# Performance work log

Hardware: AMD Instinct MI355X
Metric: run time of the kernel (lower is better)

The kernel has to match this reference:

```python
import jax, jax.numpy as jnp
import numpy as np
import math

D_MODEL = 512
N_HEAD = 8
D_HEAD = 64
N_LAYER = 12
D_FF = 2048
EMB_SIZES = [32, 128, 256, 256, 32, 64]
N_TOKEN = [32, 32, 90, 70, 8, 8]
EPS_ATTN = 1e-6
EPS_LN = 1e-5


def _pos_encoding(seq, d):
    pos = np.arange(seq, dtype=np.float32)[:, None]
    div = np.exp(np.arange(0, d, 2, dtype=np.float32) * (-math.log(10000.0) / d))
    pe = np.zeros((seq, d), np.float32)
    pe[:, 0::2] = np.sin(pos * div)
    pe[:, 1::2] = np.cos(pos * div)
    return jnp.asarray(pe)


def _layernorm(x, g, b):
    mu = jnp.mean(x, axis=-1, keepdims=True)
    var = jnp.var(x, axis=-1, keepdims=True)
    return (x - mu) * jax.lax.rsqrt(var + EPS_LN) * g + b


def _phi(x):
    # elu(x) + 1
    return jnp.where(x > 0, x + 1.0, jnp.exp(x))


def _causal_linear_attention(h, wq, bq, wk, bk, wv, bv, wo, bo):
    B, S, _ = h.shape
    q = _phi((h @ wq + bq).reshape(B, S, N_HEAD, D_HEAD))
    k = _phi((h @ wk + bk).reshape(B, S, N_HEAD, D_HEAD))
    v = (h @ wv + bv).reshape(B, S, N_HEAD, D_HEAD)
    # cumulative K^T V state: [B,S,H,D,D]
    kv = jnp.cumsum(k[..., :, None] * v[..., None, :], axis=1)
    ksum = jnp.cumsum(k, axis=1)
    z = 1.0 / (jnp.einsum('bshd,bshd->bsh', q, ksum) + EPS_ATTN)
    out = jnp.einsum('bshd,bshde->bshe', q, kv) * z[..., None]
    return out.reshape(B, S, D_MODEL) @ wo + bo


def _forward(x, emb_bar, emb_position, emb_pitch, emb_duration, emb_type, emb_emotion,
             in_w, in_b, wq, bq, wk, bk, wv, bv, wo, bo,
             ln1_g, ln1_b, w1, b1, w2, b2, ln2_g, ln2_b,
             lnf_g, lnf_b, proj_emo_w, proj_emo_b):
    tables = [emb_bar, emb_position, emb_pitch, emb_duration, emb_type, emb_emotion]
    embs = jnp.concatenate(
        [jnp.take(t, x[..., i], axis=0) * math.sqrt(EMB_SIZES[i]) for i, t in enumerate(tables)],
        axis=-1)  # [B,S,768]
    h = embs @ in_w + in_b
    S = h.shape[1]
    h = h + _pos_encoding(S, D_MODEL)[None, :, :]  # dropout is identity in eval

    def layer(hc, p):
        (wq_, bq_, wk_, bk_, wv_, bv_, wo_, bo_,
         g1, be1, w1_, b1_, w2_, b2_, g2, be2) = p
        hc = hc + _causal_linear_attention(hc, wq_, bq_, wk_, bk_, wv_, bv_, wo_, bo_)
        hc = _layernorm(hc, g1, be1)
        y = jax.nn.gelu(hc @ w1_ + b1_, approximate=False) @ w2_ + b2_
        hc = _layernorm(hc + y, g2, be2)
        return hc, None

    params = (wq, bq, wk, bk, wv, bv, wo, bo, ln1_g, ln1_b, w1, b1, w2, b2, ln2_g, ln2_b)
    h, _ = jax.lax.scan(layer, h, params)
    h = _layernorm(h, lnf_g, lnf_b)  # final encoder norm
    y_emotion = h @ proj_emo_w + proj_emo_b
    return h, y_emotion


def setup_inputs() -> dict:
    key = jax.random.key(0)
    ks = jax.random.split(key, 16)
    B, S = 1, 1024
    x = jax.random.randint(ks[0], (B, S, 6), 0, 8)

    def lin(k, fin, fout):
        k1, k2 = jax.random.split(k)
        lim = 1.0 / np.sqrt(fin)
        return (jax.random.uniform(k1, (fin, fout), minval=-lim, maxval=lim),
                jax.random.uniform(k2, (fout,), minval=-lim, maxval=lim))

    def stack_lin(k, fin, fout):
        kk = jax.random.split(k, N_LAYER)
        ws, bs = zip(*[lin(kk[i], fin, fout) for i in range(N_LAYER)])
        return jnp.stack(ws), jnp.stack(bs)

    def stack_ln(val):
        return jnp.full((N_LAYER, D_MODEL), val, jnp.float32)

    inp = {'x': x}
    names = ['emb_bar', 'emb_position', 'emb_pitch', 'emb_duration', 'emb_type', 'emb_emotion']
    for i, n in enumerate(names):
        inp[n] = jax.random.normal(jax.random.fold_in(ks[1], i), (N_TOKEN[i], EMB_SIZES[i])) * 0.02
    inp['in_w'], inp['in_b'] = lin(ks[2], sum(EMB_SIZES), D_MODEL)
    inp['wq'], inp['bq'] = stack_lin(ks[3], D_MODEL, D_MODEL)
    inp['wk'], inp['bk'] = stack_lin(ks[4], D_MODEL, D_MODEL)
    inp['wv'], inp['bv'] = stack_lin(ks[5], D_MODEL, D_MODEL)
    inp['wo'], inp['bo'] = stack_lin(ks[6], D_MODEL, D_MODEL)
    inp['ln1_g'], inp['ln1_b'] = stack_ln(1.0), stack_ln(0.0)
    inp['w1'], inp['b1'] = stack_lin(ks[7], D_MODEL, D_FF)
    inp['w2'], inp['b2'] = stack_lin(ks[8], D_FF, D_MODEL)
    inp['ln2_g'], inp['ln2_b'] = stack_ln(1.0), stack_ln(0.0)
    inp['lnf_g'], inp['lnf_b'] = jnp.ones((D_MODEL,)), jnp.zeros((D_MODEL,))
    inp['proj_emo_w'], inp['proj_emo_b'] = lin(ks[9], D_MODEL, N_TOKEN[5])
    return inp


def reference(x, emb_bar, emb_position, emb_pitch, emb_duration, emb_type, emb_emotion,
              in_w, in_b, wq, bq, wk, bk, wv, bv, wo, bo,
              ln1_g, ln1_b, w1, b1, w2, b2, ln2_g, ln2_b,
              lnf_g, lnf_b, proj_emo_w, proj_emo_b):
    return _forward(x, emb_bar, emb_position, emb_pitch, emb_duration, emb_type, emb_emotion,
                    in_w, in_b, wq, bq, wk, bk, wv, bv, wo, bo,
                    ln1_g, ln1_b, w1, b1, w2, b2, ln2_g, ln2_b,
                    lnf_g, lnf_b, proj_emo_w, proj_emo_b)
```

## Files before the change

kernel.cpp:

```cpp
#include <hip/hip_runtime.h>
#include <hip/hip_bf16.h>
#include <math.h>


#define S_LEN 1024
#define DM 512
#define NH 8
#define DH 64
#define DFF 2048
#define NLAYER 12
#define CHUNK 64
#define NCH (S_LEN / CHUNK)

#define ACT_NONE 0
#define ACT_PHI  1
#define ACT_GELU 2

typedef short s16x8 __attribute__((ext_vector_type(8)));
typedef float f32x4 __attribute__((ext_vector_type(4)));

__device__ __forceinline__ short f2bf(float x) {
    __hip_bfloat16 h = __float2bfloat16(x);
    return *reinterpret_cast<short*>(&h);
}

__device__ __forceinline__ void fma4(f32x4& a, float s, const f32x4 v) {
    a.x = fmaf(s, v.x, a.x); a.y = fmaf(s, v.y, a.y);
    a.z = fmaf(s, v.z, a.z); a.w = fmaf(s, v.w, a.w);
}

__device__ __forceinline__ void tile_barrier() {
    asm volatile("s_waitcnt lgkmcnt(0)" ::: "memory");
    __builtin_amdgcn_s_barrier();
    asm volatile("" ::: "memory");
}

__global__ __launch_bounds__(256) void embed_kernel(
    const int* __restrict__ x,
    const float* __restrict__ t0, const float* __restrict__ t1,
    const float* __restrict__ t2, const float* __restrict__ t3,
    const float* __restrict__ t4, const float* __restrict__ t5,
    short* __restrict__ EMBb)
{
    int s = blockIdx.x;
    __shared__ int xi[6];
    if (threadIdx.x < 6) xi[threadIdx.x] = x[s * 6 + threadIdx.x];
    __syncthreads();
    for (int j = threadIdx.x; j < 768; j += 256) {
        int i, off, width; const float* t; float sc;
        if (j < 32)       { i = 0; off = 0;   t = t0; sc = 5.656854249f;  width = 32;  }
        else if (j < 160) { i = 1; off = 32;  t = t1; sc = 11.3137085f;   width = 128; }
        else if (j < 416) { i = 2; off = 160; t = t2; sc = 16.0f;         width = 256; }
        else if (j < 672) { i = 3; off = 416; t = t3; sc = 16.0f;         width = 256; }
        else if (j < 704) { i = 4; off = 672; t = t4; sc = 5.656854249f;  width = 32;  }
        else              { i = 5; off = 704; t = t5; sc = 8.0f;          width = 64;  }
        EMBb[s * 768 + j] = f2bf(t[xi[i] * width + (j - off)] * sc);
    }
}

__global__ __launch_bounds__(256) void transpose_w(
    const float* __restrict__ in, short* __restrict__ out, int K, int N)
{
    __shared__ short t[64][66];
    const int b = blockIdx.z;
    const int n0 = blockIdx.x * 64, k0 = blockIdx.y * 64;
    const float* ip = in + (size_t)b * K * N;
    short* op = out + (size_t)b * K * N;
    const int c = threadIdx.x & 63, r0 = (threadIdx.x >> 6) * 16;
    #pragma unroll
    for (int i = 0; i < 16; ++i)
        t[c][r0 + i] = f2bf(ip[(size_t)(k0 + r0 + i) * N + n0 + c]);
    __syncthreads();
    #pragma unroll
    for (int i = 0; i < 16; ++i)
        op[(size_t)(n0 + r0 + i) * K + k0 + c] = t[r0 + i][c];
}

__device__ __forceinline__ float apply_act(float v, int act) {
    if (act == ACT_PHI)       return (v > 0.0f) ? (v + 1.0f) : expf(v);
    else if (act == ACT_GELU) return 0.5f * v * (1.0f + erff(v * 0.70710678118654752f));
    return v;
}


__device__ __forceinline__ void ldswr64(short* lds, int srow, int scolb,
                                        const s16x8 r[2])
{
    const int bc = scolb ^ ((srow & 7) << 4);
    #pragma unroll
    for (int p = 0; p < 2; ++p)
        *(s16x8*)((char*)lds + (p * 32 + srow) * 128 + bc) = r[p];
}

__device__ __forceinline__ void compute64(
    const short* __restrict__ As, const short* __restrict__ Bs,
    int wr, int wc, int l15, int q, f32x4 acc[2][2])
{
    #pragma unroll
    for (int kh = 0; kh < 2; ++kh) {
        const int kb = kh * 64 + q * 16;
        s16x8 a[2], b[2];
        #pragma unroll
        for (int m = 0; m < 2; ++m) {
            int row = wr * 32 + m * 16 + l15;
            a[m] = *(const s16x8*)((const char*)As + row * 128 + (kb ^ ((row & 7) << 4)));
        }
        #pragma unroll
        for (int n = 0; n < 2; ++n) {
            int row = wc * 32 + n * 16 + l15;
            b[n] = *(const s16x8*)((const char*)Bs + row * 128 + (kb ^ ((row & 7) << 4)));
        }
        #pragma unroll
        for (int m = 0; m < 2; ++m)
            #pragma unroll
            for (int n = 0; n < 2; ++n)
                acc[m][n] = __builtin_amdgcn_mfma_f32_16x16x32_bf16(
                    a[m], b[n], acc[m][n], 0, 0, 0);
    }
}

__global__ __launch_bounds__(256) void gemm64(
    const short* __restrict__ A, const short* __restrict__ BT,
    const float* __restrict__ bias, const float* __restrict__ resid,
    float* __restrict__ Cf, short* __restrict__ Cbf,
    int N, int K, int act, int add_pe, int zparts)
{
    __shared__ short As[2][4096];
    __shared__ short Bs[2][4096];
    const int tid = threadIdx.x;
    const int row0 = blockIdx.y * 64, col0 = blockIdx.x * 64;
    const int z = blockIdx.z;
    const int Kz = K / zparts;
    const int kbase = z * Kz;
    const int w = tid >> 6, lane = tid & 63, q = lane >> 4, l15 = lane & 15;
    const int wr = w >> 1, wc = w & 1;
    const int nt = Kz >> 6;

    const int srow = tid >> 3;
    const int scolb = (tid & 7) * 16;
    const char* gA = (const char*)(A  + (size_t)(row0 + srow) * K + kbase) + scolb;
    const char* gB = (const char*)(BT + (size_t)(col0 + srow) * K + kbase) + scolb;
    const size_t rstep = (size_t)32 * K * 2;

    s16x8 ra[2], rb[2];
    #pragma unroll
    for (int p = 0; p < 2; ++p) {
        ra[p] = *(const s16x8*)(gA + p * rstep);
        rb[p] = *(const s16x8*)(gB + p * rstep);
    }
    ldswr64(As[0], srow, scolb, ra);
    ldswr64(Bs[0], srow, scolb, rb);
    if (nt > 1) {
        #pragma unroll
        for (int p = 0; p < 2; ++p) {
            ra[p] = *(const s16x8*)(gA + p * rstep + 128);
            rb[p] = *(const s16x8*)(gB + p * rstep + 128);
        }
    }
    tile_barrier();

    f32x4 acc[2][2] = {};
    int cur = 0;
    for (int t = 0; t < nt; ++t) {
        if (t + 1 < nt) {
            ldswr64(As[cur ^ 1], srow, scolb, ra);
            ldswr64(Bs[cur ^ 1], srow, scolb, rb);
        }
        if (t + 2 < nt) {
            size_t ko = (size_t)(t + 2) * 128;
            #pragma unroll
            for (int p = 0; p < 2; ++p) {
                ra[p] = *(const s16x8*)(gA + p * rstep + ko);
                rb[p] = *(const s16x8*)(gB + p * rstep + ko);
            }
        }
        compute64(As[cur], Bs[cur], wr, wc, l15, q, acc);
        tile_barrier();
        cur ^= 1;
    }

    if (zparts > 1 && Cf) Cf += (size_t)z * S_LEN * N;

    const int rbase = row0 + wr * 32 + q * 4;
    const int cbase = col0 + wc * 32 + l15;
    #pragma unroll
    for (int n = 0; n < 2; ++n) {
        int c = cbase + n * 16;
        float bia = (z == 0) ? bias[c] : 0.0f;
        #pragma unroll
        for (int m = 0; m < 2; ++m) {
            #pragma unroll
            for (int rg = 0; rg < 4; ++rg) {
                int r = rbase + m * 16 + rg;
                float v = apply_act(acc[m][n][rg] + bia, act);
                if (resid) v += resid[(size_t)r * N + c];
                if (add_pe) {
                    float freq = expf((float)(c & ~1) * (-9.210340371976184f / 512.0f));
                    float ang = (float)r * freq;
                    v += (c & 1) ? cosf(ang) : sinf(ang);
                }
                if (Cf)  Cf[(size_t)r * N + c] = v;
                if (Cbf) Cbf[(size_t)r * N + c] = f2bf(v);
            }
        }
    }
}

__global__ __launch_bounds__(256) void qkv64(
    const short* __restrict__ Hb,
    const short* __restrict__ qT, const short* __restrict__ kT, const short* __restrict__ vT,
    const float* __restrict__ bq, const float* __restrict__ bk, const float* __restrict__ bv,
    float* __restrict__ Qb, float* __restrict__ Kb, float* __restrict__ Vb)
{
    __shared__ short As[2][4096];
    __shared__ short Bs[2][4096];
    const int sel  = blockIdx.x >> 3;
    const int col0 = (blockIdx.x & 7) * 64;
    const int row0 = blockIdx.y * 64;
    const short* BT   = (sel == 0) ? qT : (sel == 1) ? kT : vT;
    const float* bias = (sel == 0) ? bq : (sel == 1) ? bk : bv;
    float* C          = (sel == 0) ? Qb : (sel == 1) ? Kb : Vb;
    const bool phi = (sel < 2);

    const int tid = threadIdx.x;
    const int w = tid >> 6, lane = tid & 63, q = lane >> 4, l15 = lane & 15;
    const int wr = w >> 1, wc = w & 1;

    const int srow = tid >> 3;
    const int scolb = (tid & 7) * 16;
    const char* gA = (const char*)(Hb + (size_t)(row0 + srow) * DM) + scolb;
    const char* gB = (const char*)(BT + (size_t)(col0 + srow) * DM) + scolb;
    const size_t rstep = (size_t)32 * DM * 2;

    s16x8 ra[2], rb[2];
    #pragma unroll
    for (int p = 0; p < 2; ++p) {
        ra[p] = *(const s16x8*)(gA + p * rstep);
        rb[p] = *(const s16x8*)(gB + p * rstep);
    }
    ldswr64(As[0], srow, scolb, ra);
    ldswr64(Bs[0], srow, scolb, rb);
    #pragma unroll
    for (int p = 0; p < 2; ++p) {
        ra[p] = *(const s16x8*)(gA + p * rstep + 128);
        rb[p] = *(const s16x8*)(gB + p * rstep + 128);
    }
    tile_barrier();

    f32x4 acc[2][2] = {};
    int cur = 0;
    for (int t = 0; t < 8; ++t) {
        if (t + 1 < 8) {
            ldswr64(As[cur ^ 1], srow, scolb, ra);
            ldswr64(Bs[cur ^ 1], srow, scolb, rb);
        }
        if (t + 2 < 8) {
            size_t ko = (size_t)(t + 2) * 128;
            #pragma unroll
            for (int p = 0; p < 2; ++p) {
                ra[p] = *(const s16x8*)(gA + p * rstep + ko);
                rb[p] = *(const s16x8*)(gB + p * rstep + ko);
            }
        }
        compute64(As[cur], Bs[cur], wr, wc, l15, q, acc);
        tile_barrier();
        cur ^= 1;
    }

    const int rbase = row0 + wr * 32 + q * 4;
    const int cbase = col0 + wc * 32 + l15;
    #pragma unroll
    for (int n = 0; n < 2; ++n) {
        int c = cbase + n * 16;
        float bia = bias[c];
        #pragma unroll
        for (int m = 0; m < 2; ++m) {
            #pragma unroll
            for (int rg = 0; rg < 4; ++rg) {
                int r = rbase + m * 16 + rg;
                float v = acc[m][n][rg] + bia;
                if (phi) v = (v > 0.0f) ? (v + 1.0f) : expf(v);
                C[(size_t)r * DM + c] = v;
            }
        }
    }
}

__global__ __launch_bounds__(256) void chunk_stats_kernel(
    const float* __restrict__ Kb, const float* __restrict__ Vb,
    float* __restrict__ KVC, float* __restrict__ KSC)
{
    const int h = blockIdx.x >> 4, c = blockIdx.x & 15;
    const int tid = threadIdx.x;
    __shared__ float Ks[64][68];
    __shared__ float Vs[64][68];
    #pragma unroll
    for (int it = 0; it < 4; ++it) {
        int j = tid + it * 256;
        int r = j >> 4, d0 = (j & 15) * 4;
        size_t g = (size_t)(c * CHUNK + r) * DM + h * 64 + d0;
        *(f32x4*)(&Ks[r][d0]) = *(const f32x4*)(Kb + g);
        *(f32x4*)(&Vs[r][d0]) = *(const f32x4*)(Vb + g);
    }
    __syncthreads();
    const int di = (tid >> 4) * 4, ei = (tid & 15) * 4;
    f32x4 a0 = {}, a1 = {}, a2 = {}, a3 = {}, ks = {};
    #pragma unroll 8
    for (int t = 0; t < 64; ++t) {
        f32x4 kk = *(const f32x4*)(&Ks[t][di]);
        f32x4 vv = *(const f32x4*)(&Vs[t][ei]);
        fma4(a0, kk.x, vv); fma4(a1, kk.y, vv);
        fma4(a2, kk.z, vv); fma4(a3, kk.w, vv);
        ks += kk;
    }
    float* out = KVC + (size_t)(c * NH + h) * 4096;
    *(f32x4*)(out + (size_t)(di + 0) * 64 + ei) = a0;
    *(f32x4*)(out + (size_t)(di + 1) * 64 + ei) = a1;
    *(f32x4*)(out + (size_t)(di + 2) * 64 + ei) = a2;
    *(f32x4*)(out + (size_t)(di + 3) * 64 + ei) = a3;
    if ((tid & 15) == 0)
        *(f32x4*)(KSC + (size_t)(c * NH + h) * 64 + di) = ks;
}

__global__ __launch_bounds__(256) void attn_out_kernel(
    const float* __restrict__ Qb, const float* __restrict__ Kb,
    const float* __restrict__ Vb, const float* __restrict__ KVC,
    const float* __restrict__ KSC, short* __restrict__ Ab)
{
    const int h = blockIdx.x >> 4, c = blockIdx.x & 15;
    const int tid = threadIdx.x;
    __shared__ float Qt[64][68];
    __shared__ float Kt[64][68];
    __shared__ float Vs[64][68];
    __shared__ float Ms[64][68];
    __shared__ float St[64][68];
    __shared__ float KSs[64];

    {
        f32x4 macc[4] = {};
        for (int cp = 0; cp < c; ++cp) {
            const float* src = KVC + (size_t)(cp * NH + h) * 4096;
            #pragma unroll
            for (int it = 0; it < 4; ++it)
                macc[it] += *(const f32x4*)(src + (size_t)(tid + it * 256) * 4);
        }
        #pragma unroll
        for (int it = 0; it < 4; ++it) {
            int j = tid + it * 256;
            *(f32x4*)(&Ms[j >> 4][(j & 15) * 4]) = macc[it];
        }
        if (tid < 64) {
            float s = 0.0f;
            for (int cp = 0; cp < c; ++cp)
                s += KSC[(size_t)(cp * NH + h) * 64 + tid];
            KSs[tid] = s;
        }
    }
    #pragma unroll
    for (int it = 0; it < 4; ++it) {
        int j = tid + it * 256;
        int r = j >> 4, d0 = (j & 15) * 4;
        size_t g = (size_t)(c * CHUNK + r) * DM + h * 64 + d0;
        f32x4 q = *(const f32x4*)(Qb + g);
        f32x4 k = *(const f32x4*)(Kb + g);
        f32x4 v = *(const f32x4*)(Vb + g);
        Qt[d0 + 0][r] = q.x; Qt[d0 + 1][r] = q.y; Qt[d0 + 2][r] = q.z; Qt[d0 + 3][r] = q.w;
        Kt[d0 + 0][r] = k.x; Kt[d0 + 1][r] = k.y; Kt[d0 + 2][r] = k.z; Kt[d0 + 3][r] = k.w;
        *(f32x4*)(&Vs[r][d0]) = v;
    }
    __syncthreads();

    const int si = tid >> 4, ti = tid & 15;
    const int s0 = si * 4, t0 = ti * 4;

    f32x4 accO0 = {}, accO1 = {}, accO2 = {}, accO3 = {};
    f32x4 den = {};
    #pragma unroll 8
    for (int d = 0; d < 64; ++d) {
        f32x4 qv = *(const f32x4*)(&Qt[d][s0]);
        f32x4 mv = *(const f32x4*)(&Ms[d][t0]);
        float ks = KSs[d];
        fma4(accO0, qv.x, mv); fma4(accO1, qv.y, mv);
        fma4(accO2, qv.z, mv); fma4(accO3, qv.w, mv);
        fma4(den, ks, qv);
    }

    f32x4 p0 = {}, p1 = {}, p2 = {}, p3 = {};
    if (ti <= si) {
        #pragma unroll 8
        for (int d = 0; d < 64; ++d) {
            f32x4 qv = *(const f32x4*)(&Qt[d][s0]);
            f32x4 kv = *(const f32x4*)(&Kt[d][t0]);
            fma4(p0, qv.x, kv); fma4(p1, qv.y, kv);
            fma4(p2, qv.z, kv); fma4(p3, qv.w, kv);
        }
        if (ti == si) {
            p0.y = 0.0f; p0.z = 0.0f; p0.w = 0.0f;
            p1.z = 0.0f; p1.w = 0.0f;
            p2.w = 0.0f;
        }
    }
    St[t0 + 0][s0 + 0] = p0.x; St[t0 + 1][s0 + 0] = p0.y;
    St[t0 + 2][s0 + 0] = p0.z; St[t0 + 3][s0 + 0] = p0.w;
    St[t0 + 0][s0 + 1] = p1.x; St[t0 + 1][s0 + 1] = p1.y;
    St[t0 + 2][s0 + 1] = p1.z; St[t0 + 3][s0 + 1] = p1.w;
    St[t0 + 0][s0 + 2] = p2.x; St[t0 + 1][s0 + 2] = p2.y;
    St[t0 + 2][s0 + 2] = p2.z; St[t0 + 3][s0 + 2] = p2.w;
    St[t0 + 0][s0 + 3] = p3.x; St[t0 + 1][s0 + 3] = p3.y;
    St[t0 + 2][s0 + 3] = p3.z; St[t0 + 3][s0 + 3] = p3.w;
    __syncthreads();

    const int tmax = s0 + 4;
    #pragma unroll 4
    for (int t2 = 0; t2 < tmax; ++t2) {
        f32x4 sv = *(const f32x4*)(&St[t2][s0]);
        f32x4 vv = *(const f32x4*)(&Vs[t2][t0]);
        fma4(accO0, sv.x, vv); fma4(accO1, sv.y, vv);
        fma4(accO2, sv.z, vv); fma4(accO3, sv.w, vv);
        den += sv;
    }

    short* op = Ab + (size_t)(c * CHUNK + s0) * DM + h * 64 + t0;
    {
        float z = 1.0f / (den.x + 1e-6f);
        short4 o; o.x = f2bf(accO0.x * z); o.y = f2bf(accO0.y * z);
        o.z = f2bf(accO0.z * z); o.w = f2bf(accO0.w * z);
        *reinterpret_cast<short4*>(op) = o;
    }
    {
        float z = 1.0f / (den.y + 1e-6f);
        short4 o; o.x = f2bf(accO1.x * z); o.y = f2bf(accO1.y * z);
        o.z = f2bf(accO1.z * z); o.w = f2bf(accO1.w * z);
        *reinterpret_cast<short4*>(op + DM) = o;
    }
    {
        float z = 1.0f / (den.z + 1e-6f);
        short4 o; o.x = f2bf(accO2.x * z); o.y = f2bf(accO2.y * z);
        o.z = f2bf(accO2.z * z); o.w = f2bf(accO2.w * z);
        *reinterpret_cast<short4*>(op + 2 * DM) = o;
    }
    {
        float z = 1.0f / (den.w + 1e-6f);
        short4 o; o.x = f2bf(accO3.x * z); o.y = f2bf(accO3.y * z);
        o.z = f2bf(accO3.z * z); o.w = f2bf(accO3.w * z);
        *reinterpret_cast<short4*>(op + 3 * DM) = o;
    }
}

__device__ __forceinline__ float block_reduce_sum(float v, float* smem)
{
    #pragma unroll
    for (int o = 32; o > 0; o >>= 1) v += __shfl_down(v, o, 64);
    int w = threadIdx.x >> 6;
    if ((threadIdx.x & 63) == 0) smem[w] = v;
    __syncthreads();
    v = smem[0] + smem[1] + smem[2] + smem[3];
    __syncthreads();
    return v;
}

__global__ __launch_bounds__(256) void ln_kernel(
    const float* __restrict__ X, const float* __restrict__ X2,
    const float* __restrict__ resid,
    const float* __restrict__ g, const float* __restrict__ b,
    float* __restrict__ O, short* __restrict__ Ob)
{
    __shared__ float red[4];
    const int row = blockIdx.x;
    const size_t base = (size_t)row * DM;
    const int t = threadIdx.x;
    float v0 = X[base + t], v1 = X[base + t + 256];
    if (X2)    { v0 += X2[base + t];    v1 += X2[base + t + 256]; }
    if (resid) { v0 += resid[base + t]; v1 += resid[base + t + 256]; }
    float mean = block_reduce_sum(v0 + v1, red) * (1.0f / 512.0f);
    float d0 = v0 - mean, d1 = v1 - mean;
    float var = block_reduce_sum(d0 * d0 + d1 * d1, red) * (1.0f / 512.0f);
    float rs = 1.0f / sqrtf(var + 1e-5f);
    float o0 = d0 * rs * g[t] + b[t];
    float o1 = d1 * rs * g[t + 256] + b[t + 256];
    O[base + t]       = o0;
    O[base + t + 256] = o1;
    if (Ob) {
        Ob[base + t]       = f2bf(o0);
        Ob[base + t + 256] = f2bf(o1);
    }
}

__global__ __launch_bounds__(256) void proj_emo_kernel(
    const float* __restrict__ HF, const float* __restrict__ pw,
    const float* __restrict__ pb, float* __restrict__ out)
{
    __shared__ float pws[4096];
    for (int i = threadIdx.x; i < 4096; i += 256) pws[i] = pw[i];
    __syncthreads();
    int idx = blockIdx.x * 256 + threadIdx.x;
    int r = idx >> 3, e = idx & 7;
    float acc = pb[e];
    const float* h = HF + (size_t)r * DM;
    for (int d = 0; d < DM; d += 4) {
        f32x4 hv = *(const f32x4*)(h + d);
        acc += hv.x * pws[(d + 0) * 8 + e] + hv.y * pws[(d + 1) * 8 + e]
             + hv.z * pws[(d + 2) * 8 + e] + hv.w * pws[(d + 3) * 8 + e];
    }
    out[idx] = acc;
}

extern "C" void kernel_launch(void* const* d_in, const int* in_sizes, int n_in,
                              void* d_out, int out_size, void* d_ws, size_t ws_size,
                              hipStream_t stream)
{
    const int*   x    = (const int*)d_in[0];
    const float* e0   = (const float*)d_in[1];
    const float* e1   = (const float*)d_in[2];
    const float* e2   = (const float*)d_in[3];
    const float* e3   = (const float*)d_in[4];
    const float* e4   = (const float*)d_in[5];
    const float* e5   = (const float*)d_in[6];
    const float* in_w = (const float*)d_in[7];
    const float* in_b = (const float*)d_in[8];
    const float* wq   = (const float*)d_in[9];
    const float* bq   = (const float*)d_in[10];
    const float* wk   = (const float*)d_in[11];
    const float* bk   = (const float*)d_in[12];
    const float* wv   = (const float*)d_in[13];
    const float* bv   = (const float*)d_in[14];
    const float* wo   = (const float*)d_in[15];
    const float* bo   = (const float*)d_in[16];
    const float* g1   = (const float*)d_in[17];
    const float* be1  = (const float*)d_in[18];
    const float* w1   = (const float*)d_in[19];
    const float* b1   = (const float*)d_in[20];
    const float* w2   = (const float*)d_in[21];
    const float* b2   = (const float*)d_in[22];
    const float* g2   = (const float*)d_in[23];
    const float* be2  = (const float*)d_in[24];
    const float* gf   = (const float*)d_in[25];
    const float* bfin = (const float*)d_in[26];
    const float* pw   = (const float*)d_in[27];
    const float* pb   = (const float*)d_in[28];
    float* outp = (float*)d_out;

    float* ws = (float*)d_ws;
    float* H    = ws;
    float* Y    = ws + 524288;
    float* Y2   = ws + 1048576;
    float* Qb   = ws + 1572864;
    float* Kb   = ws + 2097152;
    float* Vb   = ws + 2621440;
    float* KVC  = ws + 3145728;
    float* KSC  = ws + 3670016;
    short* sb   = (short*)(ws + 3678208);
    short* Hb   = sb;
    short* Ab   = sb + 524288;
    short* FFb  = sb + 1048576;
    short* EMBb = FFb;
    short* inT  = sb + 3145728;
    short* qT   = inT + 393216;
    short* kT   = qT + 3145728;
    short* vT   = kT + 3145728;
    short* oT   = vT + 3145728;
    short* w1T  = oT + 3145728;
    short* w2T  = w1T + 12582912;

    const dim3 blk256(256);

    transpose_w<<<dim3(8, 12, 1),  blk256, 0, stream>>>(in_w, inT, 768, DM);
    transpose_w<<<dim3(8, 8, 12),  blk256, 0, stream>>>(wq, qT, DM, DM);
    transpose_w<<<dim3(8, 8, 12),  blk256, 0, stream>>>(wk, kT, DM, DM);
    transpose_w<<<dim3(8, 8, 12),  blk256, 0, stream>>>(wv, vT, DM, DM);
    transpose_w<<<dim3(8, 8, 12),  blk256, 0, stream>>>(wo, oT, DM, DM);
    transpose_w<<<dim3(32, 8, 12), blk256, 0, stream>>>(w1, w1T, DM, DFF);
    transpose_w<<<dim3(8, 32, 12), blk256, 0, stream>>>(w2, w2T, DFF, DM);

    embed_kernel<<<S_LEN, blk256, 0, stream>>>(x, e0, e1, e2, e3, e4, e5, EMBb);
    gemm64<<<dim3(8, 16, 1), blk256, 0, stream>>>(EMBb, inT, in_b, nullptr,
                                                  H, Hb, DM, 768, ACT_NONE, 1, 1);

    for (int l = 0; l < NLAYER; ++l) {
        const short* qT_l = qT + (size_t)l * DM * DM;
        const short* kT_l = kT + (size_t)l * DM * DM;
        const short* vT_l = vT + (size_t)l * DM * DM;
        const short* oT_l = oT + (size_t)l * DM * DM;
        const short* w1T_l = w1T + (size_t)l * DM * DFF;
        const short* w2T_l = w2T + (size_t)l * DM * DFF;
        const float* bq_l = bq + l * DM;  const float* bk_l = bk + l * DM;
        const float* bv_l = bv + l * DM;  const float* bo_l = bo + l * DM;
        const float* b1_l = b1 + l * DFF; const float* b2_l = b2 + l * DM;

        qkv64<<<dim3(24, 16), blk256, 0, stream>>>(Hb, qT_l, kT_l, vT_l,
                                                   bq_l, bk_l, bv_l, Qb, Kb, Vb);

        chunk_stats_kernel<<<NCH * NH, blk256, 0, stream>>>(Kb, Vb, KVC, KSC);
        attn_out_kernel<<<NCH * NH, blk256, 0, stream>>>(Qb, Kb, Vb, KVC, KSC, Ab);

        gemm64<<<dim3(8, 16, 2), blk256, 0, stream>>>(Ab, oT_l, bo_l, nullptr,
                                                      Y, nullptr, DM, DM, ACT_NONE, 0, 2);
        ln_kernel<<<S_LEN, blk256, 0, stream>>>(Y, Y2, H,
                                                g1 + l * DM, be1 + l * DM, H, Hb);

        gemm64<<<dim3(32, 16, 1), blk256, 0, stream>>>(Hb, w1T_l, b1_l, nullptr,
                                                       nullptr, FFb, DFF, DM, ACT_GELU, 0, 1);
        gemm64<<<dim3(8, 16, 2), blk256, 0, stream>>>(FFb, w2T_l, b2_l, nullptr,
                                                      Y, nullptr, DM, DFF, ACT_NONE, 0, 2);
        ln_kernel<<<S_LEN, blk256, 0, stream>>>(Y, Y2, H,
                                                g2 + l * DM, be2 + l * DM, H, Hb);
    }

    ln_kernel<<<S_LEN, blk256, 0, stream>>>(H, nullptr, nullptr, gf, bfin, outp, nullptr);
    proj_emo_kernel<<<8192 / 256, blk256, 0, stream>>>(outp, pw, pb, outp + 524288);
}
```

Before: 1.057 ms.

## Use single-wave LayerNorm, merge QKVO weight transposes, reorder GEMM pipeline loop

LayerNorm now runs one 64-thread wave per row with vectorized float4 loads and xor-shuffle reductions, replacing the 256-thread block reduction and its LDS barriers. The four per-layer attention weight transposes are merged into one launch. The GEMM k-loops now compute before writing the next LDS buffer and skip the final barrier. The LDS write into the other buffer right after compute relies on the earlier barrier having ordered it against reads of that buffer, which is a subtle synchronisation risk.

```diff
diff --git a/kernel.cpp b/kernel.cpp
--- a/kernel.cpp
+++ b/kernel.cpp
@@ -76,6 +76,30 @@
         op[(size_t)(n0 + r0 + i) * K + k0 + c] = t[r0 + i][c];
 }
 
+__global__ __launch_bounds__(256) void transpose4_w(
+    const float* __restrict__ wA, const float* __restrict__ wB,
+    const float* __restrict__ wC, const float* __restrict__ wD,
+    short* __restrict__ oA, short* __restrict__ oB,
+    short* __restrict__ oC, short* __restrict__ oD)
+{
+    __shared__ short t[64][66];
+    const int zz = blockIdx.z;
+    const int which = zz & 3, b = zz >> 2;
+    const float* in = (which == 0) ? wA : (which == 1) ? wB : (which == 2) ? wC : wD;
+    short* out      = (which == 0) ? oA : (which == 1) ? oB : (which == 2) ? oC : oD;
+    const int n0 = blockIdx.x * 64, k0 = blockIdx.y * 64;
+    const float* ip = in + (size_t)b * DM * DM;
+    short* op = out + (size_t)b * DM * DM;
+    const int c = threadIdx.x & 63, r0 = (threadIdx.x >> 6) * 16;
+    #pragma unroll
+    for (int i = 0; i < 16; ++i)
+        t[c][r0 + i] = f2bf(ip[(size_t)(k0 + r0 + i) * DM + n0 + c]);
+    __syncthreads();
+    #pragma unroll
+    for (int i = 0; i < 16; ++i)
+        op[(size_t)(n0 + r0 + i) * DM + k0 + c] = t[r0 + i][c];
+}
+
 __device__ __forceinline__ float apply_act(float v, int act) {
     if (act == ACT_PHI)       return (v > 0.0f) ? (v + 1.0f) : expf(v);
     else if (act == ACT_GELU) return 0.5f * v * (1.0f + erff(v * 0.70710678118654752f));
@@ -162,20 +186,20 @@
     f32x4 acc[2][2] = {};
     int cur = 0;
     for (int t = 0; t < nt; ++t) {
+        compute64(As[cur], Bs[cur], wr, wc, l15, q, acc);
         if (t + 1 < nt) {
             ldswr64(As[cur ^ 1], srow, scolb, ra);
             ldswr64(Bs[cur ^ 1], srow, scolb, rb);
-        }
-        if (t + 2 < nt) {
-            size_t ko = (size_t)(t + 2) * 128;
-            #pragma unroll
-            for (int p = 0; p < 2; ++p) {
-                ra[p] = *(const s16x8*)(gA + p * rstep + ko);
-                rb[p] = *(const s16x8*)(gB + p * rstep + ko);
+            if (t + 2 < nt) {
+                size_t ko = (size_t)(t + 2) * 128;
+                #pragma unroll
+                for (int p = 0; p < 2; ++p) {
+                    ra[p] = *(const s16x8*)(gA + p * rstep + ko);
+                    rb[p] = *(const s16x8*)(gB + p * rstep + ko);
+                }
             }
-        }
-        compute64(As[cur], Bs[cur], wr, wc, l15, q, acc);
-        tile_barrier();
+            tile_barrier();
+        }
         cur ^= 1;
     }
 
@@ -250,20 +274,20 @@
     f32x4 acc[2][2] = {};
     int cur = 0;
     for (int t = 0; t < 8; ++t) {
+        compute64(As[cur], Bs[cur], wr, wc, l15, q, acc);
         if (t + 1 < 8) {
             ldswr64(As[cur ^ 1], srow, scolb, ra);
             ldswr64(Bs[cur ^ 1], srow, scolb, rb);
-        }
-        if (t + 2 < 8) {
-            size_t ko = (size_t)(t + 2) * 128;
-            #pragma unroll
-            for (int p = 0; p < 2; ++p) {
-                ra[p] = *(const s16x8*)(gA + p * rstep + ko);
-                rb[p] = *(const s16x8*)(gB + p * rstep + ko);
+            if (t + 2 < 8) {
+                size_t ko = (size_t)(t + 2) * 128;
+                #pragma unroll
+                for (int p = 0; p < 2; ++p) {
+                    ra[p] = *(const s16x8*)(gA + p * rstep + ko);
+                    rb[p] = *(const s16x8*)(gB + p * rstep + ko);
+                }
             }
-        }
-        compute64(As[cur], Bs[cur], wr, wc, l15, q, acc);
-        tile_barrier();
+            tile_barrier();
+        }
         cur ^= 1;
     }
 
@@ -447,42 +471,48 @@
     }
 }
 
-__device__ __forceinline__ float block_reduce_sum(float v, float* smem)
-{
-    #pragma unroll
-    for (int o = 32; o > 0; o >>= 1) v += __shfl_down(v, o, 64);
-    int w = threadIdx.x >> 6;
-    if ((threadIdx.x & 63) == 0) smem[w] = v;
-    __syncthreads();
-    v = smem[0] + smem[1] + smem[2] + smem[3];
-    __syncthreads();
-    return v;
-}
-
-__global__ __launch_bounds__(256) void ln_kernel(
+__global__ __launch_bounds__(64) void ln_kernel64(
     const float* __restrict__ X, const float* __restrict__ X2,
     const float* __restrict__ resid,
     const float* __restrict__ g, const float* __restrict__ b,
     float* __restrict__ O, short* __restrict__ Ob)
 {
-    __shared__ float red[4];
     const int row = blockIdx.x;
     const size_t base = (size_t)row * DM;
     const int t = threadIdx.x;
-    float v0 = X[base + t], v1 = X[base + t + 256];
-    if (X2)    { v0 += X2[base + t];    v1 += X2[base + t + 256]; }
-    if (resid) { v0 += resid[base + t]; v1 += resid[base + t + 256]; }
-    float mean = block_reduce_sum(v0 + v1, red) * (1.0f / 512.0f);
-    float d0 = v0 - mean, d1 = v1 - mean;
-    float var = block_reduce_sum(d0 * d0 + d1 * d1, red) * (1.0f / 512.0f);
+    const int i0 = 4 * t, i1 = 256 + 4 * t;
+    f32x4 v0 = *(const f32x4*)(X + base + i0);
+    f32x4 v1 = *(const f32x4*)(X + base + i1);
+    if (X2) {
+        v0 += *(const f32x4*)(X2 + base + i0);
+        v1 += *(const f32x4*)(X2 + base + i1);
+    }
+    if (resid) {
+        v0 += *(const f32x4*)(resid + base + i0);
+        v1 += *(const f32x4*)(resid + base + i1);
+    }
+    float s = v0.x + v0.y + v0.z + v0.w + v1.x + v1.y + v1.z + v1.w;
+    #pragma unroll
+    for (int m = 1; m < 64; m <<= 1) s += __shfl_xor(s, m, 64);
+    float mean = s * (1.0f / 512.0f);
+    f32x4 d0 = v0 - mean, d1 = v1 - mean;
+    float ss = d0.x * d0.x + d0.y * d0.y + d0.z * d0.z + d0.w * d0.w
+             + d1.x * d1.x + d1.y * d1.y + d1.z * d1.z + d1.w * d1.w;
+    #pragma unroll
+    for (int m = 1; m < 64; m <<= 1) ss += __shfl_xor(ss, m, 64);
+    float var = ss * (1.0f / 512.0f);
     float rs = 1.0f / sqrtf(var + 1e-5f);
-    float o0 = d0 * rs * g[t] + b[t];
-    float o1 = d1 * rs * g[t + 256] + b[t + 256];
-    O[base + t]       = o0;
-    O[base + t + 256] = o1;
+    f32x4 g0 = *(const f32x4*)(g + i0), g1v = *(const f32x4*)(g + i1);
+    f32x4 b0 = *(const f32x4*)(b + i0), b1v = *(const f32x4*)(b + i1);
+    f32x4 o0 = d0 * rs * g0 + b0;
+    f32x4 o1 = d1 * rs * g1v + b1v;
+    *(f32x4*)(O + base + i0) = o0;
+    *(f32x4*)(O + base + i1) = o1;
     if (Ob) {
-        Ob[base + t]       = f2bf(o0);
-        Ob[base + t + 256] = f2bf(o1);
+        short4 s0; s0.x = f2bf(o0.x); s0.y = f2bf(o0.y); s0.z = f2bf(o0.z); s0.w = f2bf(o0.w);
+        short4 s1; s1.x = f2bf(o1.x); s1.y = f2bf(o1.y); s1.z = f2bf(o1.z); s1.w = f2bf(o1.w);
+        *reinterpret_cast<short4*>(Ob + base + i0) = s0;
+        *reinterpret_cast<short4*>(Ob + base + i1) = s1;
     }
 }
 
@@ -562,13 +592,11 @@
     short* w1T  = oT + 3145728;
     short* w2T  = w1T + 12582912;
 
-    const dim3 blk256(256);
+    const dim3 blk256(256), blk64(64);
 
     transpose_w<<<dim3(8, 12, 1),  blk256, 0, stream>>>(in_w, inT, 768, DM);
-    transpose_w<<<dim3(8, 8, 12),  blk256, 0, stream>>>(wq, qT, DM, DM);
-    transpose_w<<<dim3(8, 8, 12),  blk256, 0, stream>>>(wk, kT, DM, DM);
-    transpose_w<<<dim3(8, 8, 12),  blk256, 0, stream>>>(wv, vT, DM, DM);
-    transpose_w<<<dim3(8, 8, 12),  blk256, 0, stream>>>(wo, oT, DM, DM);
+    transpose4_w<<<dim3(8, 8, 48), blk256, 0, stream>>>(wq, wk, wv, wo,
+                                                        qT, kT, vT, oT);
     transpose_w<<<dim3(32, 8, 12), blk256, 0, stream>>>(w1, w1T, DM, DFF);
     transpose_w<<<dim3(8, 32, 12), blk256, 0, stream>>>(w2, w2T, DFF, DM);
 
@@ -595,17 +623,17 @@
 
         gemm64<<<dim3(8, 16, 2), blk256, 0, stream>>>(Ab, oT_l, bo_l, nullptr,
                                                       Y, nullptr, DM, DM, ACT_NONE, 0, 2);
-        ln_kernel<<<S_LEN, blk256, 0, stream>>>(Y, Y2, H,
-                                                g1 + l * DM, be1 + l * DM, H, Hb);
+        ln_kernel64<<<S_LEN, blk64, 0, stream>>>(Y, Y2, H,
+                                                 g1 + l * DM, be1 + l * DM, H, Hb);
 
         gemm64<<<dim3(32, 16, 1), blk256, 0, stream>>>(Hb, w1T_l, b1_l, nullptr,
                                                        nullptr, FFb, DFF, DM, ACT_GELU, 0, 1);
         gemm64<<<dim3(8, 16, 2), blk256, 0, stream>>>(FFb, w2T_l, b2_l, nullptr,
                                                       Y, nullptr, DM, DFF, ACT_NONE, 0, 2);
-        ln_kernel<<<S_LEN, blk256, 0, stream>>>(Y, Y2, H,
-                                                g2 + l * DM, be2 + l * DM, H, Hb);
-    }
-
-    ln_kernel<<<S_LEN, blk256, 0, stream>>>(H, nullptr, nullptr, gf, bfin, outp, nullptr);
+        ln_kernel64<<<S_LEN, blk64, 0, stream>>>(Y, Y2, H,
+                                                 g2 + l * DM, be2 + l * DM, H, Hb);
+    }
+
+    ln_kernel64<<<S_LEN, blk64, 0, stream>>>(H, nullptr, nullptr, gf, bfin, outp, nullptr);
     proj_emo_kernel<<<8192 / 256, blk256, 0, stream>>>(outp, pw, pb, outp + 524288);
 }
```

Result: no change. 1.049 ms (-0.8%).
